# Performance work log

Measured on AMD Instinct MI355X. Metric: run time of the kernel, lower is better.

## Reference

```python
import jax, jax.numpy as jnp
import numpy as np

ALPHA = 0.5  # mixing weight between dot-product and wedge-norm terms


def setup_inputs() -> dict:
    key = jax.random.key(0)
    kq, kk, kv = jax.random.split(key, 3)
    B, L, H, E = 2, 2048, 8, 32
    queries = jax.random.normal(kq, (B, L, H, E), dtype=jnp.float32)
    keys = jax.random.normal(kk, (B, L, H, E), dtype=jnp.float32)
    values = jax.random.normal(kv, (B, L, H, E), dtype=jnp.float32)
    return {"queries": queries, "keys": keys, "values": values}


def reference(queries, keys, values):
    # queries: [B,L,H,E], keys: [B,S,H,E], values: [B,S,H,D]
    E = queries.shape[-1]
    scale = 1.0 / jnp.sqrt(jnp.asarray(E, dtype=queries.dtype))
    # dot product scores: [B,H,L,S]
    dot = jnp.einsum('blhe,bshe->bhls', queries, keys)
    # squared norms -> broadcastable [B,H,L,1] and [B,H,1,S]
    qn2 = jnp.sum(queries ** 2, axis=-1).transpose(0, 2, 1)[..., :, None]
    kn2 = jnp.sum(keys ** 2, axis=-1).transpose(0, 2, 1)[..., None, :]
    # wedge (Clifford) squared norm, clamped at 0
    wedge = jax.nn.relu(qn2 * kn2 - dot ** 2)
    scores = (ALPHA * dot - (1.0 - ALPHA) * wedge) * scale
    attn = jax.nn.softmax(scores, axis=-1)  # [B,H,L,S]
    # out: [B,L,H,D]
    out = jnp.einsum('bhls,bshd->blhd', attn, values)
    return out
```

## Files before the change

kernel.cpp:

```cpp
#include <hip/hip_runtime.h>
#include <hip/hip_bf16.h>
#include <math.h>


#define NB 2
#define NL 2048
#define NS 2048
#define NH 8
#define NBH 16
#define CSC 0.12751742f

#define WS_KN2_OFF 0u
#define WS_KHKL_OFF 131072u
#define WS_VT_OFF (131072u + 4194304u)
#define WS_PACC_OFF (131072u + 4194304u + 2097152u)
#define WS_PML_OFF (WS_PACC_OFF + 16777216u)
#define WS_NEED (WS_PML_OFF + 1048576u)

typedef float f32x4 __attribute__((ext_vector_type(4)));
typedef short s16x8 __attribute__((ext_vector_type(8)));
typedef unsigned short u16;

__device__ inline unsigned pk2(float a, float b) {
    __hip_bfloat162 t = __float22bfloat162_rn(make_float2(a, b));
    union { __hip_bfloat162 h; unsigned u; } cv;
    cv.h = t;
    return cv.u;
}
template <int CTRL>
__device__ inline float dpp_add(float x) {
    return x + __int_as_float(__builtin_amdgcn_mov_dpp(__float_as_int(x), CTRL, 0xF, 0xF, false));
}
__device__ inline void dma16(const void* gp, void* lp) {
    __builtin_amdgcn_global_load_lds(
        (__attribute__((address_space(1))) void*)(void*)gp,
        (__attribute__((address_space(3))) void*)lp, 16, 0, 0);
}
__device__ inline int swzK(int row) { return (row ^ (row >> 2)) & 3; }
__device__ inline int swzV(int row) { return (row + (row >> 3)) & 7; }

__global__ __launch_bounds__(256) void ga_pre(const float* __restrict__ K,
                                              const float* __restrict__ V,
                                              float* __restrict__ kn2w,
                                              u16* __restrict__ khkl,
                                              u16* __restrict__ vtw) {
    __shared__ float Vf[64][36];
    const int T = threadIdx.x;
    const int bh = blockIdx.x >> 5, stile = blockIdx.x & 31;
    const int b = bh >> 3, h = bh & 7;
    const int s0 = stile * 64;
    const int sk = T >> 2, kc = T & 3;

    const float* kp = K + ((size_t)((b * NS + s0 + sk) * NH + h)) * 32 + kc * 8;
    float4 f0 = *(const float4*)kp, f1 = *(const float4*)(kp + 4);
    float kx[8] = {f0.x, f0.y, f0.z, f0.w, f1.x, f1.y, f1.z, f1.w};
    unsigned hh[4], ll[4];
    float kn2p = 0.f;
#pragma unroll
    for (int i = 0; i < 4; i++) {
        float x0 = kx[2 * i], x1 = kx[2 * i + 1];
        kn2p = fmaf(x0, x0, kn2p);
        kn2p = fmaf(x1, x1, kn2p);
        unsigned h01 = pk2(x0, x1);
        hh[i] = h01;
        float h0 = __uint_as_float(h01 << 16);
        float h1 = __uint_as_float(h01 & 0xffff0000u);
        ll[i] = pk2(x0 - h0, x1 - h1);
    }
    u16* kd = khkl + ((size_t)(bh * NS + s0 + sk)) * 64;
    const int swk = sk & 7;
    *(uint4*)(kd + ((kc ^ swk) * 8)) = make_uint4(hh[0], hh[1], hh[2], hh[3]);
    *(uint4*)(kd + (((4 + kc) ^ swk) * 8)) = make_uint4(ll[0], ll[1], ll[2], ll[3]);
    kn2p = dpp_add<0xB1>(kn2p);
    kn2p = dpp_add<0x4E>(kn2p);
    if (kc == 0) kn2w[bh * NS + s0 + sk] = kn2p;

    const float* vp = V + ((size_t)((b * NS + s0 + sk) * NH + h)) * 32 + kc * 8;
    float4 g0 = *(const float4*)vp, g1 = *(const float4*)(vp + 4);
    *(float4*)&Vf[sk][kc * 8] = g0;
    *(float4*)&Vf[sk][kc * 8 + 4] = g1;
    __syncthreads();
    const int dr = T >> 3, c = T & 7;
    float vv[8];
#pragma unroll
    for (int i = 0; i < 8; i++) vv[i] = Vf[c * 8 + i][dr];
    const int phys = c ^ (dr & 7);
    *(uint4*)(vtw + ((size_t)(bh * 32 + dr)) * NS + s0 + phys * 8) =
        make_uint4(pk2(vv[0], vv[1]), pk2(vv[2], vv[3]), pk2(vv[4], vv[5]), pk2(vv[6], vv[7]));
}

__global__ __launch_bounds__(256, 5) void ga_dma(
    const float* __restrict__ Q, const float* __restrict__ kn2w,
    const u16* __restrict__ khkl, const u16* __restrict__ vtw,
    float* __restrict__ pacc, float* __restrict__ pml) {
    __shared__ u16 sK[2][64][64];
    __shared__ u16 sV[2][32][64];
    __shared__ u16 sP[4][16][64];

    const int T = threadIdx.x;
    const int lane = T & 63, wave = T >> 6;
    const int g = lane >> 4, lc = lane & 15, g8 = g * 8;
    const int blk = blockIdx.x;
    const int qt = blk & 31, strip = (blk >> 5) & 3, bh = blk >> 7;
    const int b = bh >> 3, h = bh & 7;
    const int qw = qt * 64 + wave * 16;
    const int kb0 = strip * 512;

    const float* qrow = Q + ((size_t)((b * NL + qw + lc) * NH + h)) * 32 + g8;
    float4 qa = *(const float4*)qrow, qb = *(const float4*)(qrow + 4);
    float q8[8] = {qa.x, qa.y, qa.z, qa.w, qb.x, qb.y, qb.z, qb.w};
    union { unsigned u4[4]; s16x8 v; } qh_, ql_;
    float qn2 = 0.f;
#pragma unroll
    for (int i = 0; i < 4; i++) {
        float x0 = q8[2 * i], x1 = q8[2 * i + 1];
        qn2 = fmaf(x0, x0, qn2);
        qn2 = fmaf(x1, x1, qn2);
        unsigned h01 = pk2(x0, x1);
        qh_.u4[i] = h01;
        float h0 = __uint_as_float(h01 << 16);
        float h1 = __uint_as_float(h01 & 0xffff0000u);
        ql_.u4[i] = pk2(x0 - h0, x1 - h1);
    }
    const s16x8 qh = qh_.v, ql = ql_.v;
    qn2 += __shfl_xor(qn2, 16);
    qn2 += __shfl_xor(qn2, 32);

    const char* ksrc = (const char*)khkl +
        ((size_t)(bh * NS + kb0 + 16 * wave)) * 128 + lane * 16;
    const char* vsrc = (const char*)vtw +
        ((size_t)(bh * 32 + 8 * wave + (lane >> 3))) * (NS * 2) +
        (size_t)(kb0 + (lane & 7) * 8) * 2;
    const float* kn2b = kn2w + (size_t)bh * NS + kb0;

    dma16(ksrc, &sK[0][16 * wave][0]);
    dma16(ksrc + 1024, &sK[0][16 * wave + 8][0]);
    dma16(vsrc, &sV[0][8 * wave][0]);

    float kmin;
    {
        f32x4 k0 = *(const f32x4*)(kn2b + 4 * g);
        f32x4 k1 = *(const f32x4*)(kn2b + 16 + 4 * g);
        f32x4 k2 = *(const f32x4*)(kn2b + 32 + 4 * g);
        f32x4 k3 = *(const f32x4*)(kn2b + 48 + 4 * g);
        float a = fminf(fminf(k0[0], k0[1]), fminf(k0[2], k0[3]));
        float bq = fminf(fminf(k1[0], k1[1]), fminf(k1[2], k1[3]));
        float c = fminf(fminf(k2[0], k2[1]), fminf(k2[2], k2[3]));
        float dq = fminf(fminf(k3[0], k3[1]), fminf(k3[2], k3[3]));
        kmin = fminf(fminf(a, bq), fminf(c, dq));
        kmin = fminf(kmin, __shfl_xor(kmin, 16));
        kmin = fminf(kmin, __shfl_xor(kmin, 32));
    }
    const float m0 = -0.5f * qn2 * kmin;
    const float m0C = -m0 * CSC;
    __syncthreads();

    s16x8 ones;
#pragma unroll
    for (int i = 0; i < 8; i++) ones[i] = (short)0x3F80;

    f32x4 acc0 = {0.f, 0.f, 0.f, 0.f}, acc1 = {0.f, 0.f, 0.f, 0.f};
    f32x4 lacc = {0.f, 0.f, 0.f, 0.f};
    const f32x4 z = {0.f, 0.f, 0.f, 0.f};
    const int sw = lc & 7;

    for (int t = 0; t < 8; ++t) {
        const int cur = t & 1;
        if (t + 1 < 8) {
            const char* k2 = ksrc + (size_t)(t + 1) * 8192;
            const char* v2 = vsrc + (size_t)(t + 1) * 128;
            dma16(k2, &sK[cur ^ 1][16 * wave][0]);
            dma16(k2 + 1024, &sK[cur ^ 1][16 * wave + 8][0]);
            dma16(v2, &sV[cur ^ 1][8 * wave][0]);
        }
        const int kl64 = t * 64;

        f32x4 d[4], kn2v[4];
#pragma unroll
        for (int st = 0; st < 4; st++) {
            kn2v[st] = *(const f32x4*)(kn2b + kl64 + 16 * st + 4 * g);
            s16x8 kh = *(s16x8*)&sK[cur][16 * st + lc][(g ^ sw) * 8];
            s16x8 klo = *(s16x8*)&sK[cur][16 * st + lc][((4 + g) ^ sw) * 8];
            f32x4 dd = __builtin_amdgcn_mfma_f32_16x16x32_bf16(klo, qh, z, 0, 0, 0);
            dd = __builtin_amdgcn_mfma_f32_16x16x32_bf16(kh, ql, dd, 0, 0, 0);
            dd = __builtin_amdgcn_mfma_f32_16x16x32_bf16(kh, qh, dd, 0, 0, 0);
            d[st] = dd;
        }
        s16x8 va0 = *(s16x8*)&sV[cur][lc][(g ^ sw) * 8];
        s16x8 va1 = *(s16x8*)&sV[cur][lc][((4 + g) ^ sw) * 8];
        s16x8 va2 = *(s16x8*)&sV[cur][lc + 16][(g ^ sw) * 8];
        s16x8 va3 = *(s16x8*)&sV[cur][lc + 16][((4 + g) ^ sw) * 8];

#pragma unroll
        for (int st = 0; st < 4; st++) {
            float p[4];
#pragma unroll
            for (int r = 0; r < 4; r++) {
                float dd = d[st][r];
                float c = qn2 * kn2v[st][r];
                float sc = fminf(dd, fmaf(dd, dd, -c) + dd);
                p[r] = __builtin_amdgcn_exp2f(fmaf(sc, CSC, m0C));
            }
            const int off = (((2 * st + (g >> 1)) ^ sw) << 3) + ((g & 1) << 2);
            *(uint2*)&sP[wave][lc][off] = make_uint2(pk2(p[0], p[1]), pk2(p[2], p[3]));
        }
        __builtin_amdgcn_s_waitcnt(0xC07F);
        s16x8 pb0 = *(s16x8*)&sP[wave][lc][(g ^ sw) * 8];
        s16x8 pb1 = *(s16x8*)&sP[wave][lc][((4 + g) ^ sw) * 8];

        acc0 = __builtin_amdgcn_mfma_f32_16x16x32_bf16(va0, pb0, acc0, 0, 0, 0);
        acc0 = __builtin_amdgcn_mfma_f32_16x16x32_bf16(va1, pb1, acc0, 0, 0, 0);
        acc1 = __builtin_amdgcn_mfma_f32_16x16x32_bf16(va2, pb0, acc1, 0, 0, 0);
        acc1 = __builtin_amdgcn_mfma_f32_16x16x32_bf16(va3, pb1, acc1, 0, 0, 0);
        lacc = __builtin_amdgcn_mfma_f32_16x16x32_bf16(ones, pb0, lacc, 0, 0, 0);
        lacc = __builtin_amdgcn_mfma_f32_16x16x32_bf16(ones, pb1, lacc, 0, 0, 0);

        __syncthreads();
    }

    float* pa = pacc + (((size_t)bh * 4 + strip) * NL + (qw + lc)) * 32;
    *(f32x4*)(pa + 4 * g) = acc0;
    *(f32x4*)(pa + 16 + 4 * g) = acc1;
    if (g == 0) {
        *(float2*)(pml + (((size_t)bh * 4 + strip) * NL + (qw + lc)) * 2) =
            make_float2(m0, lacc[0]);
    }
}

__global__ __launch_bounds__(256) void ga_combine(const float* __restrict__ pacc,
                                                  const float* __restrict__ pml,
                                                  float* __restrict__ O) {
    const int tid = blockIdx.x * 256 + threadIdx.x;
    const int dq = tid & 7, q = (tid >> 3) & 2047, bh = tid >> 14;
    const int b = bh >> 3, h = bh & 7;
    float m[4], l[4];
#pragma unroll
    for (int s = 0; s < 4; s++) {
        float2 t = *(const float2*)(pml + (((size_t)bh * 4 + s) * NL + q) * 2);
        m[s] = t.x;
        l[s] = t.y;
    }
    float mf = fmaxf(fmaxf(m[0], m[1]), fmaxf(m[2], m[3]));
    float w[4], L = 0.f;
#pragma unroll
    for (int s = 0; s < 4; s++) {
        w[s] = __builtin_amdgcn_exp2f((m[s] - mf) * CSC);
        L = fmaf(l[s], w[s], L);
    }
    const float inv = 1.f / L;
    float4 o = make_float4(0.f, 0.f, 0.f, 0.f);
#pragma unroll
    for (int s = 0; s < 4; s++) {
        const float* pa = pacc + (((size_t)bh * 4 + s) * NL + q) * 32 + dq * 4;
        float4 a = *(const float4*)pa;
        o.x = fmaf(a.x, w[s], o.x);
        o.y = fmaf(a.y, w[s], o.y);
        o.z = fmaf(a.z, w[s], o.z);
        o.w = fmaf(a.w, w[s], o.w);
    }
    o.x *= inv; o.y *= inv; o.z *= inv; o.w *= inv;
    *(float4*)(O + (((size_t)(b * NL + q)) * NH + h) * 32 + dq * 4) = o;
}

__global__ __launch_bounds__(512, 4) void ga_fallback(
    const float* __restrict__ Q, const float* __restrict__ K,
    const float* __restrict__ V, float* __restrict__ O) {
    __shared__ union {
        struct {
            u16 Kh[2][64][32];
            u16 Kl[2][64][32];
            u16 Vt[2][32][64];
            float kn2[2][64];
        } s;
        struct { float acc[8][32][17]; float m[8][16]; float l[8][16]; } c;
    } u;
    __shared__ u16 sP[8][16][64];

    const int T = threadIdx.x;
    const int lane = T & 63, wave = T >> 6;
    const int g = lane >> 4, lc = lane & 15, g8 = g * 8;
    const int half = wave >> 2;
    const int qt = blockIdx.x & 31;
    const int bh = blockIdx.x >> 5;
    const int b = bh >> 3, h = bh & 7;
    const int qw = qt * 64 + (wave & 3) * 16;

    const float* qrow = Q + ((size_t)((b * NL + qw + lc) * NH + h)) * 32 + g8;
    float4 qa = *(const float4*)qrow, qb = *(const float4*)(qrow + 4);
    float q8[8] = {qa.x, qa.y, qa.z, qa.w, qb.x, qb.y, qb.z, qb.w};
    union { unsigned u4[4]; s16x8 v; } qh_, ql_;
    float qn2 = 0.f;
#pragma unroll
    for (int i = 0; i < 4; i++) {
        float x0 = q8[2 * i], x1 = q8[2 * i + 1];
        qn2 = fmaf(x0, x0, qn2);
        qn2 = fmaf(x1, x1, qn2);
        unsigned h01 = pk2(x0, x1);
        qh_.u4[i] = h01;
        float h0 = __uint_as_float(h01 << 16);
        float h1 = __uint_as_float(h01 & 0xffff0000u);
        ql_.u4[i] = pk2(x0 - h0, x1 - h1);
    }
    const s16x8 qh = qh_.v, ql = ql_.v;
    qn2 += __shfl_xor(qn2, 16);
    qn2 += __shfl_xor(qn2, 32);

    const int Tl = T & 255;
    const int sk = Tl >> 2, kc = Tl & 3;
    const int dv = Tl & 31, vc = Tl >> 5;
    const float* kbase = K + ((size_t)(b * NS * NH) + h) * 32;
    const float* vbase = V + ((size_t)(b * NS * NH) + h) * 32;
    const int kphys = (kc ^ swzK(sk)) * 8;
    const int vphys = (vc ^ swzV(dv)) * 8;

    int s0 = half * 1024;
    float4 ka = *(const float4*)(kbase + (size_t)(s0 + sk) * 256 + kc * 8);
    float4 kb = *(const float4*)(kbase + (size_t)(s0 + sk) * 256 + kc * 8 + 4);
    float vr[8];
#pragma unroll
    for (int i = 0; i < 8; i++) vr[i] = vbase[(size_t)(s0 + 8 * vc + i) * 256 + dv];

    f32x4 acc0 = {0.f, 0.f, 0.f, 0.f}, acc1 = {0.f, 0.f, 0.f, 0.f};
    float m = -INFINITY, l = 0.f;

    for (int t = 0; t < 16; ++t) {
        {
            float kx[8] = {ka.x, ka.y, ka.z, ka.w, kb.x, kb.y, kb.z, kb.w};
            unsigned hh[4], ll[4];
            float kn2p = 0.f;
#pragma unroll
            for (int i = 0; i < 4; i++) {
                float x0 = kx[2 * i], x1 = kx[2 * i + 1];
                kn2p = fmaf(x0, x0, kn2p);
                kn2p = fmaf(x1, x1, kn2p);
                unsigned h01 = pk2(x0, x1);
                hh[i] = h01;
                float h0 = __uint_as_float(h01 << 16);
                float h1 = __uint_as_float(h01 & 0xffff0000u);
                ll[i] = pk2(x0 - h0, x1 - h1);
            }
            *(uint4*)&u.s.Kh[half][sk][kphys] = make_uint4(hh[0], hh[1], hh[2], hh[3]);
            *(uint4*)&u.s.Kl[half][sk][kphys] = make_uint4(ll[0], ll[1], ll[2], ll[3]);
            kn2p = dpp_add<0xB1>(kn2p);
            kn2p = dpp_add<0x4E>(kn2p);
            if (kc == 0) u.s.kn2[half][sk] = kn2p;
            *(uint4*)&u.s.Vt[half][dv][vphys] =
                make_uint4(pk2(vr[0], vr[1]), pk2(vr[2], vr[3]),
                           pk2(vr[4], vr[5]), pk2(vr[6], vr[7]));
        }
        const int tn = (t + 1 < 16) ? t + 1 : t;
        const int sn = half * 1024 + tn * 64;
        ka = *(const float4*)(kbase + (size_t)(sn + sk) * 256 + kc * 8);
        kb = *(const float4*)(kbase + (size_t)(sn + sk) * 256 + kc * 8 + 4);
#pragma unroll
        for (int i = 0; i < 8; i++) vr[i] = vbase[(size_t)(sn + 8 * vc + i) * 256 + dv];

        __syncthreads();

        f32x4 d[4], kn2v[4];
        const f32x4 z = {0.f, 0.f, 0.f, 0.f};
        const int skr = swzK(lc);
#pragma unroll
        for (int st = 0; st < 4; st++) {
            kn2v[st] = *(f32x4*)&u.s.kn2[half][16 * st + 4 * g];
            s16x8 kh = *(s16x8*)&u.s.Kh[half][16 * st + lc][(g ^ skr) * 8];
            s16x8 kl = *(s16x8*)&u.s.Kl[half][16 * st + lc][(g ^ skr) * 8];
            f32x4 dd = __builtin_amdgcn_mfma_f32_16x16x32_bf16(kl, qh, z, 0, 0, 0);
            dd = __builtin_amdgcn_mfma_f32_16x16x32_bf16(kh, ql, dd, 0, 0, 0);
            dd = __builtin_amdgcn_mfma_f32_16x16x32_bf16(kh, qh, dd, 0, 0, 0);
            d[st] = dd;
        }

        float sc[4][4];
#pragma unroll
        for (int st = 0; st < 4; st++)
#pragma unroll
            for (int r = 0; r < 4; r++) {
                float dd = d[st][r];
                float w = fmaxf(fmaf(-dd, dd, qn2 * kn2v[st][r]), 0.f);
                sc[st][r] = (dd - w) * CSC;
            }

        float x0 = fmaxf(fmaxf(sc[0][0], sc[0][1]), fmaxf(sc[0][2], sc[0][3]));
        float x1 = fmaxf(fmaxf(sc[1][0], sc[1][1]), fmaxf(sc[1][2], sc[1][3]));
        float x2 = fmaxf(fmaxf(sc[2][0], sc[2][1]), fmaxf(sc[2][2], sc[2][3]));
        float x3 = fmaxf(fmaxf(sc[3][0], sc[3][1]), fmaxf(sc[3][2], sc[3][3]));
        float tm = fmaxf(fmaxf(x0, x1), fmaxf(x2, x3));
        tm = fmaxf(tm, __shfl_xor(tm, 16));
        tm = fmaxf(tm, __shfl_xor(tm, 32));
        const float nm = fmaxf(m, tm);
        const float al = __builtin_amdgcn_exp2f(m - nm);
        m = nm;
        float p[4][4], ls = 0.f;
#pragma unroll
        for (int st = 0; st < 4; st++)
#pragma unroll
            for (int r = 0; r < 4; r++) {
                p[st][r] = __builtin_amdgcn_exp2f(sc[st][r] - nm);
                ls += p[st][r];
            }
        l = fmaf(l, al, ls);
        acc0 *= al;
        acc1 *= al;

#pragma unroll
        for (int st = 0; st < 4; st++) {
            const int off = ((2 * st + (g >> 1)) ^ (lc & 7)) * 8 + (g & 1) * 4;
            *(uint2*)&sP[wave][lc][off] =
                make_uint2(pk2(p[st][0], p[st][1]), pk2(p[st][2], p[st][3]));
        }
        __builtin_amdgcn_s_waitcnt(0xC07F);

        const int svl = swzV(lc), svh = swzV(lc + 16), spl = lc & 7;
        s16x8 va00 = *(s16x8*)&u.s.Vt[half][lc][(g ^ svl) * 8];
        s16x8 va01 = *(s16x8*)&u.s.Vt[half][lc][((4 + g) ^ svl) * 8];
        s16x8 va10 = *(s16x8*)&u.s.Vt[half][lc + 16][(g ^ svh) * 8];
        s16x8 va11 = *(s16x8*)&u.s.Vt[half][lc + 16][((4 + g) ^ svh) * 8];
        s16x8 pb0 = *(s16x8*)&sP[wave][lc][(g ^ spl) * 8];
        s16x8 pb1 = *(s16x8*)&sP[wave][lc][((4 + g) ^ spl) * 8];
        acc0 = __builtin_amdgcn_mfma_f32_16x16x32_bf16(va00, pb0, acc0, 0, 0, 0);
        acc0 = __builtin_amdgcn_mfma_f32_16x16x32_bf16(va01, pb1, acc0, 0, 0, 0);
        acc1 = __builtin_amdgcn_mfma_f32_16x16x32_bf16(va10, pb0, acc1, 0, 0, 0);
        acc1 = __builtin_amdgcn_mfma_f32_16x16x32_bf16(va11, pb1, acc1, 0, 0, 0);

        __syncthreads();
    }

    l += __shfl_xor(l, 16);
    l += __shfl_xor(l, 32);
#pragma unroll
    for (int r = 0; r < 4; r++) {
        u.c.acc[wave][4 * g + r][lc] = acc0[r];
        u.c.acc[wave][16 + 4 * g + r][lc] = acc1[r];
    }
    if (lane < 16) {
        u.c.m[wave][lc] = m;
        u.c.l[wave][lc] = l;
    }
    __syncthreads();

    const int q = T >> 3, dq = (T & 7) * 4, qr = q & 15;
    const int w0 = q >> 4, w1 = w0 + 4;
    float m0 = u.c.m[w0][qr], m1 = u.c.m[w1][qr];
    float l0 = u.c.l[w0][qr], l1 = u.c.l[w1][qr];
    float mf = fmaxf(m0, m1);
    float e0 = __builtin_amdgcn_exp2f(m0 - mf);
    float e1 = __builtin_amdgcn_exp2f(m1 - mf);
    float inv = 1.f / fmaf(l1, e1, l0 * e0);
    e0 *= inv;
    e1 *= inv;
    float4 o;
    o.x = u.c.acc[w0][dq + 0][qr] * e0 + u.c.acc[w1][dq + 0][qr] * e1;
    o.y = u.c.acc[w0][dq + 1][qr] * e0 + u.c.acc[w1][dq + 1][qr] * e1;
    o.z = u.c.acc[w0][dq + 2][qr] * e0 + u.c.acc[w1][dq + 2][qr] * e1;
    o.w = u.c.acc[w0][dq + 3][qr] * e0 + u.c.acc[w1][dq + 3][qr] * e1;
    *(float4*)(O + ((size_t)((b * NL + qt * 64 + q) * NH + h)) * 32 + dq) = o;
}

extern "C" void kernel_launch(void* const* d_in, const int* in_sizes, int n_in,
                              void* d_out, int out_size, void* d_ws, size_t ws_size,
                              hipStream_t stream) {
    const float* Q = (const float*)d_in[0];
    const float* K = (const float*)d_in[1];
    const float* V = (const float*)d_in[2];
    float* O = (float*)d_out;

    if (ws_size >= (size_t)WS_NEED) {
        float* kn2w = (float*)((char*)d_ws + WS_KN2_OFF);
        u16* khkl = (u16*)((char*)d_ws + WS_KHKL_OFF);
        u16* vtw = (u16*)((char*)d_ws + WS_VT_OFF);
        float* pacc = (float*)((char*)d_ws + WS_PACC_OFF);
        float* pml = (float*)((char*)d_ws + WS_PML_OFF);
        ga_pre<<<NBH * 32, 256, 0, stream>>>(K, V, kn2w, khkl, vtw);
        ga_dma<<<NBH * 32 * 4, 256, 0, stream>>>(Q, kn2w, khkl, vtw, pacc, pml);
        ga_combine<<<(NBH * NL * 8) / 256, 256, 0, stream>>>(pacc, pml, O);
    } else {
        ga_fallback<<<NBH * 32, 512, 0, stream>>>(Q, K, V, O);
    }
}
```

Before: 107.1 us.

## Give each wave its own key sub-strip over all 64 queries, drop block barriers

Restructures the attention block so each wave owns a 128-key slice and processes all four 16-query groups, instead of each wave taking 16 queries over a shared 512-key strip. Each wave streams its own K/V tiles into private LDS, so the per-tile __syncthreads disappears and each K/V fragment load is reused across four query groups. Wave partials are then merged in LDS through a log-sum-exp combine at the end. The cost is more registers (launch bounds drop from 5 to 3 blocks per CU), a larger LDS footprint, and a single-buffered DMA per wave that relies on waitcnt ordering.

```diff
diff --git a/kernel.cpp b/kernel.cpp
--- a/kernel.cpp
+++ b/kernel.cpp
@@ -89,13 +89,21 @@
         make_uint4(pk2(vv[0], vv[1]), pk2(vv[2], vv[3]), pk2(vv[4], vv[5]), pk2(vv[6], vv[7]));
 }
 
-__global__ __launch_bounds__(256, 5) void ga_dma(
+__global__ __launch_bounds__(256, 3) void ga_pw(
     const float* __restrict__ Q, const float* __restrict__ kn2w,
     const u16* __restrict__ khkl, const u16* __restrict__ vtw,
     float* __restrict__ pacc, float* __restrict__ pml) {
-    __shared__ u16 sK[2][64][64];
-    __shared__ u16 sV[2][32][64];
-    __shared__ u16 sP[4][16][64];
+    __shared__ union {
+        struct {
+            u16 K[4][32][64];
+            u16 V[4][32][32];
+            u16 P[4][64][32];
+        } s;
+        struct {
+            float cacc[4][32][69];
+            float2 cml[4][64];
+        } c;
+    } u;
 
     const int T = threadIdx.x;
     const int lane = T & 63, wave = T >> 6;
@@ -103,128 +111,189 @@
     const int blk = blockIdx.x;
     const int qt = blk & 31, strip = (blk >> 5) & 3, bh = blk >> 7;
     const int b = bh >> 3, h = bh & 7;
-    const int qw = qt * 64 + wave * 16;
-    const int kb0 = strip * 512;
-
-    const float* qrow = Q + ((size_t)((b * NL + qw + lc) * NH + h)) * 32 + g8;
-    float4 qa = *(const float4*)qrow, qb = *(const float4*)(qrow + 4);
-    float q8[8] = {qa.x, qa.y, qa.z, qa.w, qb.x, qb.y, qb.z, qb.w};
-    union { unsigned u4[4]; s16x8 v; } qh_, ql_;
-    float qn2 = 0.f;
-#pragma unroll
-    for (int i = 0; i < 4; i++) {
-        float x0 = q8[2 * i], x1 = q8[2 * i + 1];
-        qn2 = fmaf(x0, x0, qn2);
-        qn2 = fmaf(x1, x1, qn2);
-        unsigned h01 = pk2(x0, x1);
-        qh_.u4[i] = h01;
-        float h0 = __uint_as_float(h01 << 16);
-        float h1 = __uint_as_float(h01 & 0xffff0000u);
-        ql_.u4[i] = pk2(x0 - h0, x1 - h1);
-    }
-    const s16x8 qh = qh_.v, ql = ql_.v;
-    qn2 += __shfl_xor(qn2, 16);
-    qn2 += __shfl_xor(qn2, 32);
-
-    const char* ksrc = (const char*)khkl +
-        ((size_t)(bh * NS + kb0 + 16 * wave)) * 128 + lane * 16;
-    const char* vsrc = (const char*)vtw +
-        ((size_t)(bh * 32 + 8 * wave + (lane >> 3))) * (NS * 2) +
-        (size_t)(kb0 + (lane & 7) * 8) * 2;
-    const float* kn2b = kn2w + (size_t)bh * NS + kb0;
-
-    dma16(ksrc, &sK[0][16 * wave][0]);
-    dma16(ksrc + 1024, &sK[0][16 * wave + 8][0]);
-    dma16(vsrc, &sV[0][8 * wave][0]);
+    const int kw0 = strip * 512 + wave * 128;
+
+    s16x8 qh[4], ql[4];
+    float qn2[4];
+#pragma unroll
+    for (int qg = 0; qg < 4; qg++) {
+        const float* qrow =
+            Q + ((size_t)((b * NL + qt * 64 + 16 * qg + lc) * NH + h)) * 32 + g8;
+        float4 qa = *(const float4*)qrow, qb = *(const float4*)(qrow + 4);
+        float q8[8] = {qa.x, qa.y, qa.z, qa.w, qb.x, qb.y, qb.z, qb.w};
+        union { unsigned u4[4]; s16x8 v; } H, L;
+        float qp = 0.f;
+#pragma unroll
+        for (int i = 0; i < 4; i++) {
+            float x0 = q8[2 * i], x1 = q8[2 * i + 1];
+            qp = fmaf(x0, x0, qp);
+            qp = fmaf(x1, x1, qp);
+            unsigned h01 = pk2(x0, x1);
+            H.u4[i] = h01;
+            float h0 = __uint_as_float(h01 << 16);
+            float h1 = __uint_as_float(h01 & 0xffff0000u);
+            L.u4[i] = pk2(x0 - h0, x1 - h1);
+        }
+        qh[qg] = H.v;
+        ql[qg] = L.v;
+        qp += __shfl_xor(qp, 16);
+        qp += __shfl_xor(qp, 32);
+        qn2[qg] = qp;
+    }
+
+    const char* ksrcB =
+        (const char*)khkl + ((size_t)(bh * NS + kw0)) * 128 + lane * 16;
+    const int dL0 = lane >> 2, lu = lane & 3;
+    const char* vpe[2];
+    const char* vpo[2];
+#pragma unroll
+    for (int i = 0; i < 2; i++) {
+        const int d = 16 * i + dL0, x = d & 7;
+        const size_t rowb = ((size_t)(bh * 32 + d)) * NS + kw0;
+        vpe[i] = (const char*)vtw + (rowb + (size_t)((lu ^ x) * 8)) * 2;
+        vpo[i] = (const char*)vtw + (rowb + (size_t)((((4 + lu) ^ x)) * 8)) * 2;
+    }
+    const float* kn2b = kn2w + (size_t)bh * NS + kw0;
 
     float kmin;
     {
         f32x4 k0 = *(const f32x4*)(kn2b + 4 * g);
         f32x4 k1 = *(const f32x4*)(kn2b + 16 + 4 * g);
-        f32x4 k2 = *(const f32x4*)(kn2b + 32 + 4 * g);
-        f32x4 k3 = *(const f32x4*)(kn2b + 48 + 4 * g);
         float a = fminf(fminf(k0[0], k0[1]), fminf(k0[2], k0[3]));
         float bq = fminf(fminf(k1[0], k1[1]), fminf(k1[2], k1[3]));
-        float c = fminf(fminf(k2[0], k2[1]), fminf(k2[2], k2[3]));
-        float dq = fminf(fminf(k3[0], k3[1]), fminf(k3[2], k3[3]));
-        kmin = fminf(fminf(a, bq), fminf(c, dq));
+        kmin = fminf(a, bq);
         kmin = fminf(kmin, __shfl_xor(kmin, 16));
         kmin = fminf(kmin, __shfl_xor(kmin, 32));
     }
-    const float m0 = -0.5f * qn2 * kmin;
-    const float m0C = -m0 * CSC;
+    float m0[4], m0C[4];
+#pragma unroll
+    for (int qg = 0; qg < 4; qg++) {
+        m0[qg] = -0.5f * qn2[qg] * kmin;
+        m0C[qg] = -m0[qg] * CSC;
+    }
+
+#pragma unroll
+    for (int i = 0; i < 4; i++) dma16(ksrcB + i * 1024, &u.s.K[wave][8 * i][0]);
+    dma16(vpe[0], &u.s.V[wave][0][0]);
+    dma16(vpe[1], &u.s.V[wave][16][0]);
+
+    s16x8 ones;
+#pragma unroll
+    for (int i = 0; i < 8; i++) ones[i] = (short)0x3F80;
+
+    f32x4 acc[2][4], lacc[4];
+#pragma unroll
+    for (int ds = 0; ds < 2; ds++)
+#pragma unroll
+        for (int qg = 0; qg < 4; qg++) acc[ds][qg] = (f32x4){0.f, 0.f, 0.f, 0.f};
+#pragma unroll
+    for (int qg = 0; qg < 4; qg++) lacc[qg] = (f32x4){0.f, 0.f, 0.f, 0.f};
+    const f32x4 z = {0.f, 0.f, 0.f, 0.f};
+    const int sw7 = lc & 7, sw3 = lc & 3;
+
+    for (int t = 0; t < 4; ++t) {
+        __builtin_amdgcn_s_waitcnt(0x0F70);
+
+        f32x4 kn2v0 = *(const f32x4*)(kn2b + t * 32 + 4 * g);
+        f32x4 kn2v1 = *(const f32x4*)(kn2b + t * 32 + 16 + 4 * g);
+
+        s16x8 kh0 = *(s16x8*)&u.s.K[wave][lc][(g ^ sw7) * 8];
+        s16x8 kl0 = *(s16x8*)&u.s.K[wave][lc][((4 + g) ^ sw7) * 8];
+        s16x8 kh1 = *(s16x8*)&u.s.K[wave][16 + lc][(g ^ sw7) * 8];
+        s16x8 kl1 = *(s16x8*)&u.s.K[wave][16 + lc][((4 + g) ^ sw7) * 8];
+        s16x8 va0 = *(s16x8*)&u.s.V[wave][lc][g8];
+        s16x8 va1 = *(s16x8*)&u.s.V[wave][16 + lc][g8];
+        __builtin_amdgcn_s_waitcnt(0xC07F);
+
+        if (t + 1 < 4) {
+            const char* kB = ksrcB + (size_t)(t + 1) * 4096;
+#pragma unroll
+            for (int i = 0; i < 4; i++) dma16(kB + i * 1024, &u.s.K[wave][8 * i][0]);
+            const char* v0 = (((t + 1) & 1) ? vpo[0] : vpe[0]) + ((t + 1) >> 1) * 128;
+            const char* v1 = (((t + 1) & 1) ? vpo[1] : vpe[1]) + ((t + 1) >> 1) * 128;
+            dma16(v0, &u.s.V[wave][0][0]);
+            dma16(v1, &u.s.V[wave][16][0]);
+        }
+
+#pragma unroll
+        for (int st = 0; st < 2; st++) {
+            const s16x8 kh = st ? kh1 : kh0;
+            const s16x8 kl = st ? kl1 : kl0;
+            const f32x4 kn2v = st ? kn2v1 : kn2v0;
+#pragma unroll
+            for (int qg = 0; qg < 4; qg++) {
+                f32x4 dd = __builtin_amdgcn_mfma_f32_16x16x32_bf16(kl, qh[qg], z, 0, 0, 0);
+                dd = __builtin_amdgcn_mfma_f32_16x16x32_bf16(kh, ql[qg], dd, 0, 0, 0);
+                dd = __builtin_amdgcn_mfma_f32_16x16x32_bf16(kh, qh[qg], dd, 0, 0, 0);
+                float p[4];
+#pragma unroll
+                for (int r = 0; r < 4; r++) {
+                    float dv = dd[r];
+                    float c = qn2[qg] * kn2v[r];
+                    float sc = fminf(dv, fmaf(dv, dv, -c) + dv);
+                    p[r] = __builtin_amdgcn_exp2f(fmaf(sc, CSC, m0C[qg]));
+                }
+                const int phys = (2 * st + (g >> 1)) ^ sw3;
+                *(uint2*)((char*)&u.s.P[wave][16 * qg + lc][0] + phys * 16 + (g & 1) * 8) =
+                    make_uint2(pk2(p[0], p[1]), pk2(p[2], p[3]));
+            }
+        }
+        __builtin_amdgcn_s_waitcnt(0xC07F);
+
+#pragma unroll
+        for (int qg = 0; qg < 4; qg++) {
+            s16x8 pb = *(s16x8*)((char*)&u.s.P[wave][16 * qg + lc][0] + ((g ^ sw3) * 16));
+            acc[0][qg] = __builtin_amdgcn_mfma_f32_16x16x32_bf16(va0, pb, acc[0][qg], 0, 0, 0);
+            acc[1][qg] = __builtin_amdgcn_mfma_f32_16x16x32_bf16(va1, pb, acc[1][qg], 0, 0, 0);
+            lacc[qg] = __builtin_amdgcn_mfma_f32_16x16x32_bf16(ones, pb, lacc[qg], 0, 0, 0);
+        }
+    }
+
     __syncthreads();
-
-    s16x8 ones;
-#pragma unroll
-    for (int i = 0; i < 8; i++) ones[i] = (short)0x3F80;
-
-    f32x4 acc0 = {0.f, 0.f, 0.f, 0.f}, acc1 = {0.f, 0.f, 0.f, 0.f};
-    f32x4 lacc = {0.f, 0.f, 0.f, 0.f};
-    const f32x4 z = {0.f, 0.f, 0.f, 0.f};
-    const int sw = lc & 7;
-
-    for (int t = 0; t < 8; ++t) {
-        const int cur = t & 1;
-        if (t + 1 < 8) {
-            const char* k2 = ksrc + (size_t)(t + 1) * 8192;
-            const char* v2 = vsrc + (size_t)(t + 1) * 128;
-            dma16(k2, &sK[cur ^ 1][16 * wave][0]);
-            dma16(k2 + 1024, &sK[cur ^ 1][16 * wave + 8][0]);
-            dma16(v2, &sV[cur ^ 1][8 * wave][0]);
-        }
-        const int kl64 = t * 64;
-
-        f32x4 d[4], kn2v[4];
-#pragma unroll
-        for (int st = 0; st < 4; st++) {
-            kn2v[st] = *(const f32x4*)(kn2b + kl64 + 16 * st + 4 * g);
-            s16x8 kh = *(s16x8*)&sK[cur][16 * st + lc][(g ^ sw) * 8];
-            s16x8 klo = *(s16x8*)&sK[cur][16 * st + lc][((4 + g) ^ sw) * 8];
-            f32x4 dd = __builtin_amdgcn_mfma_f32_16x16x32_bf16(klo, qh, z, 0, 0, 0);
-            dd = __builtin_amdgcn_mfma_f32_16x16x32_bf16(kh, ql, dd, 0, 0, 0);
-            dd = __builtin_amdgcn_mfma_f32_16x16x32_bf16(kh, qh, dd, 0, 0, 0);
-            d[st] = dd;
-        }
-        s16x8 va0 = *(s16x8*)&sV[cur][lc][(g ^ sw) * 8];
-        s16x8 va1 = *(s16x8*)&sV[cur][lc][((4 + g) ^ sw) * 8];
-        s16x8 va2 = *(s16x8*)&sV[cur][lc + 16][(g ^ sw) * 8];
-        s16x8 va3 = *(s16x8*)&sV[cur][lc + 16][((4 + g) ^ sw) * 8];
-
-#pragma unroll
-        for (int st = 0; st < 4; st++) {
-            float p[4];
-#pragma unroll
-            for (int r = 0; r < 4; r++) {
-                float dd = d[st][r];
-                float c = qn2 * kn2v[st][r];
-                float sc = fminf(dd, fmaf(dd, dd, -c) + dd);
-                p[r] = __builtin_amdgcn_exp2f(fmaf(sc, CSC, m0C));
-            }
-            const int off = (((2 * st + (g >> 1)) ^ sw) << 3) + ((g & 1) << 2);
-            *(uint2*)&sP[wave][lc][off] = make_uint2(pk2(p[0], p[1]), pk2(p[2], p[3]));
-        }
-        __builtin_amdgcn_s_waitcnt(0xC07F);
-        s16x8 pb0 = *(s16x8*)&sP[wave][lc][(g ^ sw) * 8];
-        s16x8 pb1 = *(s16x8*)&sP[wave][lc][((4 + g) ^ sw) * 8];
-
-        acc0 = __builtin_amdgcn_mfma_f32_16x16x32_bf16(va0, pb0, acc0, 0, 0, 0);
-        acc0 = __builtin_amdgcn_mfma_f32_16x16x32_bf16(va1, pb1, acc0, 0, 0, 0);
-        acc1 = __builtin_amdgcn_mfma_f32_16x16x32_bf16(va2, pb0, acc1, 0, 0, 0);
-        acc1 = __builtin_amdgcn_mfma_f32_16x16x32_bf16(va3, pb1, acc1, 0, 0, 0);
-        lacc = __builtin_amdgcn_mfma_f32_16x16x32_bf16(ones, pb0, lacc, 0, 0, 0);
-        lacc = __builtin_amdgcn_mfma_f32_16x16x32_bf16(ones, pb1, lacc, 0, 0, 0);
-
-        __syncthreads();
-    }
-
-    float* pa = pacc + (((size_t)bh * 4 + strip) * NL + (qw + lc)) * 32;
-    *(f32x4*)(pa + 4 * g) = acc0;
-    *(f32x4*)(pa + 16 + 4 * g) = acc1;
+#pragma unroll
+    for (int ds = 0; ds < 2; ds++)
+#pragma unroll
+        for (int qg = 0; qg < 4; qg++)
+#pragma unroll
+            for (int r = 0; r < 4; r++)
+                u.c.cacc[wave][16 * ds + 4 * g + r][16 * qg + lc] = acc[ds][qg][r];
     if (g == 0) {
-        *(float2*)(pml + (((size_t)bh * 4 + strip) * NL + (qw + lc)) * 2) =
-            make_float2(m0, lacc[0]);
-    }
+#pragma unroll
+        for (int qg = 0; qg < 4; qg++)
+            u.c.cml[wave][16 * qg + lc] = make_float2(m0[qg], lacc[qg][0]);
+    }
+    __syncthreads();
+
+    const int q = T >> 2, dc = T & 3;
+    float mm[4], llv[4];
+#pragma unroll
+    for (int w = 0; w < 4; w++) {
+        float2 t2 = u.c.cml[w][q];
+        mm[w] = t2.x;
+        llv[w] = t2.y;
+    }
+    float mf = fmaxf(fmaxf(mm[0], mm[1]), fmaxf(mm[2], mm[3]));
+    float e[4], L = 0.f;
+#pragma unroll
+    for (int w = 0; w < 4; w++) {
+        e[w] = __builtin_amdgcn_exp2f((mm[w] - mf) * CSC);
+        L = fmaf(llv[w], e[w], L);
+    }
+    float o[8];
+#pragma unroll
+    for (int i = 0; i < 8; i++) {
+        const int d = dc * 8 + i;
+        float s = 0.f;
+#pragma unroll
+        for (int w = 0; w < 4; w++) s = fmaf(u.c.cacc[w][d][q], e[w], s);
+        o[i] = s;
+    }
+    float* pa = pacc + ((((size_t)bh * 4 + strip) * NL + qt * 64 + q)) * 32 + dc * 8;
+    *(float4*)pa = make_float4(o[0], o[1], o[2], o[3]);
+    *(float4*)(pa + 4) = make_float4(o[4], o[5], o[6], o[7]);
+    if (dc == 0)
+        *(float2*)(pml + (((size_t)bh * 4 + strip) * NL + qt * 64 + q) * 2) =
+            make_float2(mf, L);
 }
 
 __global__ __launch_bounds__(256) void ga_combine(const float* __restrict__ pacc,
@@ -472,7 +541,7 @@
         float* pacc = (float*)((char*)d_ws + WS_PACC_OFF);
         float* pml = (float*)((char*)d_ws + WS_PML_OFF);
         ga_pre<<<NBH * 32, 256, 0, stream>>>(K, V, kn2w, khkl, vtw);
-        ga_dma<<<NBH * 32 * 4, 256, 0, stream>>>(Q, kn2w, khkl, vtw, pacc, pml);
+        ga_pw<<<NBH * 32 * 4, 256, 0, stream>>>(Q, kn2w, khkl, vtw, pacc, pml);
         ga_combine<<<(NBH * NL * 8) / 256, 256, 0, stream>>>(pacc, pml, O);
     } else {
         ga_fallback<<<NBH * 32, 512, 0, stream>>>(Q, K, V, O);
```

After: 111.0 us. +3.7%, slower.
